# Optimization experiments

Hardware: AMD Instinct MI355X
Metric: run time of the kernel (lower is better)

Reference implementation:

```python
import jax, jax.numpy as jnp
import numpy as np

B, S, HID = 2, 2048, 2048
NH, NKV, HD = 16, 4, 128
EPS = 1e-6
THETA = 10000.0
NEG = jnp.float32(-1e30)


def setup_inputs() -> dict:
    key = jax.random.key(0)
    ks = jax.random.split(key, 7)
    return {
        "hidden_states": jax.random.normal(ks[0], (B, S, HID), jnp.float32) * 0.02,
        "positions": jnp.broadcast_to(jnp.arange(S, dtype=jnp.int32), (B, S)),
        "Wq": jax.random.normal(ks[1], (HID, NH * HD), jnp.float32) * (HID ** -0.5),
        "Wk": jax.random.normal(ks[2], (HID, NKV * HD), jnp.float32) * (HID ** -0.5),
        "Wv": jax.random.normal(ks[3], (HID, NKV * HD), jnp.float32) * (HID ** -0.5),
        "Wc": jax.random.normal(ks[4], (NH * HD, HID), jnp.float32) * ((NH * HD) ** -0.5),
        "q_scale": jax.random.uniform(ks[5], (HD,), jnp.float32),
        "k_scale": jax.random.uniform(ks[6], (HD,), jnp.float32),
    }


def _rmsnorm(x, scale):
    # per-head RMSNorm over head_dim (nnx.RMSNorm semantics)
    return x * jax.lax.rsqrt(jnp.mean(x * x, axis=-1, keepdims=True) + EPS) * scale


def _rope_neox(x, positions):
    # x: [B, S, H, HD]; full rotary_dim == HD, neox style (split halves)
    half = HD // 2
    inv_freq = 1.0 / (THETA ** (jnp.arange(half, dtype=jnp.float32) / half))
    ang = positions[..., None].astype(jnp.float32) * inv_freq  # [B, S, half]
    cos = jnp.cos(ang)[:, :, None, :]
    sin = jnp.sin(ang)[:, :, None, :]
    x1, x2 = jnp.split(x, 2, axis=-1)
    return jnp.concatenate([x1 * cos - x2 * sin, x2 * cos + x1 * sin], axis=-1)


def reference(hidden_states, positions, Wq, Wk, Wv, Wc, q_scale, k_scale):
    q = (hidden_states @ Wq).reshape(B, S, NH, HD)
    k = (hidden_states @ Wk).reshape(B, S, NKV, HD)
    v = (hidden_states @ Wv).reshape(B, S, NKV, HD)
    q = _rmsnorm(q, q_scale)
    k = _rmsnorm(k, k_scale)
    q = _rope_neox(q, positions)
    k = _rope_neox(k, positions)
    # GQA: expand KV heads to query heads
    rep = NH // NKV
    k = jnp.repeat(k, rep, axis=2)
    v = jnp.repeat(v, rep, axis=2)
    scores = jnp.einsum("bqhd,bkhd->bhqk", q, k) * (HD ** -0.5)
    causal = jnp.tril(jnp.ones((S, S), dtype=bool))
    scores = jnp.where(causal, scores, NEG)
    probs = jax.nn.softmax(scores, axis=-1)
    attn = jnp.einsum("bhqk,bkhd->bqhd", probs, v).reshape(B, S, NH * HD)
    return attn @ Wc
```

## Files before the change

kernel.cpp:

```cpp
#include <hip/hip_runtime.h>
#include <stdint.h>

typedef unsigned short u16;
typedef unsigned int u32;
typedef __bf16 bf16x8 __attribute__((ext_vector_type(8)));
typedef float f32x4 __attribute__((ext_vector_type(4)));
typedef u32 u32x4 __attribute__((ext_vector_type(4)));

__device__ __forceinline__ u16 f2bf(float x){
  u32 u = __float_as_uint(x);
  u += 0x7FFFu + ((u >> 16) & 1u);
  return (u16)(u >> 16);
}
__device__ __forceinline__ float bf2f(u16 h){
  return __uint_as_float(((u32)h) << 16);
}
__device__ __forceinline__ u32 cvt_pk_bf16(float lo, float hi){
  u32 r;
  asm("v_cvt_pk_bf16_f32 %0, %1, %2" : "=v"(r) : "v"(lo), "v"(hi));
  return r;
}
__device__ __forceinline__ f32x4 mfma16(bf16x8 a, bf16x8 b, f32x4 c){
  return __builtin_amdgcn_mfma_f32_16x16x32_bf16(a, b, c, 0, 0, 0);
}
__device__ __forceinline__ void gload16(const void* g, const void* l){
  __builtin_amdgcn_global_load_lds(
      (__attribute__((address_space(1))) void*)(uintptr_t)g,
      (__attribute__((address_space(3))) void*)(u32)(uintptr_t)l,
      16, 0, 0);
}

__global__ void k_rope_table(float* __restrict__ ct, float* __restrict__ st){
  int idx = blockIdx.x * 256 + threadIdx.x;
  int p = idx >> 6, i = idx & 63;
  float freq = powf(10000.0f, -(float)i / 64.0f);
  float ang = (float)p * freq;
  ct[idx] = cosf(ang);
  st[idx] = sinf(ang);
}

__global__ void k_cast_bf16(const float* __restrict__ in, u16* __restrict__ out){
  int i = (blockIdx.x * 256 + threadIdx.x) * 4;
  float4 v = *(const float4*)(in + i);
  ushort4 o;
  o.x = f2bf(v.x); o.y = f2bf(v.y); o.z = f2bf(v.z); o.w = f2bf(v.w);
  *(ushort4*)(out + i) = o;
}

__global__ void k_trans_qkv(const float* __restrict__ Wq, const float* __restrict__ Wk,
                            const float* __restrict__ Wv, u16* __restrict__ out){
  __shared__ float tile[32][33];
  int nb = blockIdx.x * 32, kb = blockIdx.y * 32;
  int tx = threadIdx.x, ty = threadIdx.y;
  #pragma unroll
  for (int j = 0; j < 4; j++){
    int k = kb + ty + j*8;
    int n = nb + tx;
    float v;
    if (n < 2048)      v = Wq[(size_t)k*2048 + n];
    else if (n < 2560) v = Wk[(size_t)k*512 + (n - 2048)];
    else               v = Wv[(size_t)k*512 + (n - 2560)];
    tile[tx][ty + j*8] = v;
  }
  __syncthreads();
  #pragma unroll
  for (int j = 0; j < 4; j++){
    int n = nb + ty + j*8;
    out[(size_t)n*2048 + kb + tx] = f2bf(tile[ty + j*8][tx]);
  }
}

__global__ void k_trans_wc(const float* __restrict__ Wc, u16* __restrict__ out){
  __shared__ float tile[32][33];
  int nb = blockIdx.x * 32, kb = blockIdx.y * 32;
  int tx = threadIdx.x, ty = threadIdx.y;
  #pragma unroll
  for (int j = 0; j < 4; j++){
    tile[tx][ty + j*8] = Wc[(size_t)(kb + ty + j*8)*2048 + nb + tx];
  }
  __syncthreads();
  #pragma unroll
  for (int j = 0; j < 4; j++){
    out[(size_t)(nb + ty + j*8)*2048 + kb + tx] = f2bf(tile[ty + j*8][tx]);
  }
}

template<bool OBF>
__global__ __launch_bounds__(256) void k_gemm(const u16* __restrict__ A, const u16* __restrict__ Bt,
                                              void* __restrict__ Cv, int M, int N, int K, int nbx){
  __shared__ u16 As[2][128*32], Bs[2][128*32];
  int tid = threadIdx.x;
  int lane = tid & 63, w = tid >> 6;
  int g = lane >> 4, c16 = lane & 15;
  int wr = w >> 1, wc = w & 1;
  int chunk = gridDim.x >> 3;
  int logical = (blockIdx.x & 7) * chunk + (blockIdx.x >> 3);
  int bx = logical % nbx, by = logical / nbx;
  size_t bm = (size_t)by * 128, bn = (size_t)bx * 128;
  f32x4 zero = {0.f, 0.f, 0.f, 0.f};
  f32x4 acc[4][4];
  #pragma unroll
  for (int i=0;i<4;i++)
    #pragma unroll
    for (int j=0;j<4;j++) acc[i][j] = zero;

  int jj = (w*2)*64 + lane;
  int nt = K >> 5;
  #pragma unroll
  for (int p = 0; p < 2; p++){
    int j = jj + p*64;
    int r = j >> 2, slot = j & 3;
    gload16(A  + (bm + r)*(size_t)K + slot*8, (const char*)As[0] + (w*2+p)*1024);
    gload16(Bt + (bn + r)*(size_t)K + slot*8, (const char*)Bs[0] + (w*2+p)*1024);
  }
  asm volatile("s_waitcnt vmcnt(0)" ::: "memory");
  __builtin_amdgcn_s_barrier();

  int cur = 0;
  for (int t = 0; t < nt; ++t){
    if (t + 1 < nt){
      int k0 = (t + 1) << 5;
      #pragma unroll
      for (int p = 0; p < 2; p++){
        int j = jj + p*64;
        int r = j >> 2, slot = j & 3;
        gload16(A  + (bm + r)*(size_t)K + k0 + slot*8, (const char*)As[cur^1] + (w*2+p)*1024);
        gload16(Bt + (bn + r)*(size_t)K + k0 + slot*8, (const char*)Bs[cur^1] + (w*2+p)*1024);
      }
    }
    const u16* Ac = As[cur];
    const u16* Bc = Bs[cur];
    bf16x8 af[4], bfr[4];
    #pragma unroll
    for (int mi=0;mi<4;mi++) af[mi]  = *(const bf16x8*)&Ac[(wr*64 + mi*16 + c16)*32 + g*8];
    #pragma unroll
    for (int ni=0;ni<4;ni++) bfr[ni] = *(const bf16x8*)&Bc[(wc*64 + ni*16 + c16)*32 + g*8];
    #pragma unroll
    for (int mi=0;mi<4;mi++)
      #pragma unroll
      for (int ni=0;ni<4;ni++)
        acc[mi][ni] = mfma16(af[mi], bfr[ni], acc[mi][ni]);
    if (t + 1 < nt){
      asm volatile("s_waitcnt vmcnt(0)" ::: "memory");
      __builtin_amdgcn_s_barrier();
    }
    cur ^= 1;
  }
  #pragma unroll
  for (int mi=0;mi<4;mi++){
    #pragma unroll
    for (int ni=0;ni<4;ni++){
      #pragma unroll
      for (int r=0;r<4;r++){
        size_t row = bm + wr*64 + mi*16 + g*4 + r;
        size_t col = bn + wc*64 + ni*16 + c16;
        if (OBF) ((u16*)Cv)[row * (size_t)N + col] = f2bf(acc[mi][ni][r]);
        else     ((float*)Cv)[row * (size_t)N + col] = acc[mi][ni][r];
      }
    }
  }
}

__global__ __launch_bounds__(256) void k_norm_rope(const u16* __restrict__ qkv, const int* __restrict__ pos,
    const float* __restrict__ qsc, const float* __restrict__ ksc,
    const float* __restrict__ ct, const float* __restrict__ st,
    u16* __restrict__ qo, u16* __restrict__ ko){
  int bs = blockIdx.x;
  int hh = blockIdx.y * 4 + (threadIdx.x >> 6);
  int d = threadIdx.x & 63;
  int b = bs >> 11, s = bs & 2047;
  const u16* row = qkv + (size_t)bs * 3072 + hh * 128;
  u16 r1 = row[d], r2 = row[d + 64];
  float x1 = bf2f(r1), x2 = bf2f(r2);
  float ssq = x1*x1 + x2*x2;
  #pragma unroll
  for (int mm = 1; mm < 64; mm <<= 1) ssq += __shfl_xor(ssq, mm);
  float inv = rsqrtf(ssq * (1.0f/128.0f) + 1e-6f);
  const float* sc = (hh < 16) ? qsc : ksc;
  float y1 = x1 * inv * sc[d];
  float y2 = x2 * inv * sc[d + 64];
  int p = pos[bs];
  float c = ct[p*64 + d], sn = st[p*64 + d];
  float o1 = y1*c - y2*sn;
  float o2 = y2*c + y1*sn;
  if (hh < 16){
    o1 *= 0.08838834764831845f;
    o2 *= 0.08838834764831845f;
    size_t o = ((size_t)(b*16 + hh) * 2048 + s) * 128 + d;
    qo[o] = f2bf(o1); qo[o + 64] = f2bf(o2);
  } else {
    size_t o = ((size_t)(b*4 + (hh-16)) * 2048 + s) * 128 + d;
    ko[o] = f2bf(o1); ko[o + 64] = f2bf(o2);
  }
}

__global__ __launch_bounds__(256) void k_vtrans(const u16* __restrict__ qkv, u16* __restrict__ vt){
  __shared__ u16 tile[64][132];
  int s0 = blockIdx.x * 64, kvh = blockIdx.y, b = blockIdx.z;
  int t = threadIdx.x;
  int r = t >> 2, qd = (t & 3) * 32;
  const u16* src = qkv + ((size_t)(b*2048 + s0 + r)) * 3072 + 2560 + kvh*128 + qd;
  #pragma unroll
  for (int i = 0; i < 4; i++)
    *(uint4*)&tile[r][qd + i*8] = *(const uint4*)(src + i*8);
  __syncthreads();
  int d = t >> 1, c = (t & 1) * 32;
  u16* dst = vt + ((size_t)(b*4 + kvh) * 128 + d) * 2048 + s0 + c;
  #pragma unroll
  for (int i = 0; i < 4; i++){
    u16 tmp[8];
    #pragma unroll
    for (int j = 0; j < 8; j++) tmp[j] = tile[c + i*8 + j][d];
    *(uint4*)(dst + i*8) = *(const uint4*)tmp;
  }
}

__device__ __forceinline__ void stage_kv(int w, int lane, u16* ksb, u16* vsb,
                                         const u16* kp, const u16* vp, int c0){
  #pragma unroll
  for (int p = 0; p < 4; p++){
    int j = (w*4 + p)*64 + lane;
    int r = j >> 4, slot = j & 15;
    const u16* src = kp + (size_t)(c0 + r)*128 + ((slot ^ (r & 7)) << 3);
    gload16(src, (const char*)ksb + (w*4 + p)*1024);
  }
  #pragma unroll
  for (int p = 0; p < 4; p++){
    int j = (w*4 + p)*64 + lane;
    int r = j >> 3, slot = j & 7;
    const u16* src = vp + (size_t)r*2048 + c0 + ((slot ^ (r & 7)) << 3);
    gload16(src, (const char*)vsb + (w*4 + p)*1024);
  }
}

__device__ __forceinline__ void proc_group(f32x4 (&sacc)[4], float &m, float &l,
    f32x4 (&o)[8], int qrow, bool diag, int c0, int lane, int g, int c16,
    const u16* vsb){
  if (diag){
    #pragma unroll
    for (int nt = 0; nt < 4; nt++)
      #pragma unroll
      for (int r = 0; r < 4; r++)
        if (c0 + nt*16 + g*4 + r > qrow) sacc[nt][r] = -1e30f;
  }
  float mx = fmaxf(fmaxf(sacc[0][0], sacc[0][1]), fmaxf(sacc[0][2], sacc[0][3]));
  #pragma unroll
  for (int nt = 1; nt < 4; nt++)
    mx = fmaxf(mx, fmaxf(fmaxf(sacc[nt][0], sacc[nt][1]), fmaxf(sacc[nt][2], sacc[nt][3])));
  mx = fmaxf(mx, __shfl_xor(mx, 16));
  mx = fmaxf(mx, __shfl_xor(mx, 32));
  if (__any(mx > m + 8.f)){
    float mn = fmaxf(m, mx);
    float al = __expf(m - mn);
    m = mn; l *= al;
    float alr[4];
    #pragma unroll
    for (int r = 0; r < 4; r++) alr[r] = __shfl(al, (lane & 48) | (g*4 + r));
    #pragma unroll
    for (int dt = 0; dt < 8; dt++)
      #pragma unroll
      for (int r = 0; r < 4; r++) o[dt][r] *= alr[r];
  }
  float s = 0.f;
  #pragma unroll
  for (int nt = 0; nt < 4; nt++)
    #pragma unroll
    for (int r = 0; r < 4; r++){
      float p = __expf(sacc[nt][r] - m);
      sacc[nt][r] = p;
      s += p;
    }
  s += __shfl_xor(s, 16);
  s += __shfl_xor(s, 32);
  l += s;
  u32 pkA[4], pkB[4];
  #pragma unroll
  for (int a = 0; a < 4; a++){
    pkA[a] = cvt_pk_bf16(sacc[a][0], sacc[a][1]);
    pkB[a] = cvt_pk_bf16(sacc[a][2], sacc[a][3]);
  }
  int s0l = (((g*2    ) & 3) << 4) | c16;
  int s1l = (((g*2 + 1) & 3) << 4) | c16;
  bool hi = (g & 2) != 0;
  u32 v0A[4], v0B[4], v1A[4], v1B[4];
  #pragma unroll
  for (int a = 0; a < 4; a++){
    v0A[a] = (u32)__shfl((int)pkA[a], s0l);
    v0B[a] = (u32)__shfl((int)pkB[a], s0l);
    v1A[a] = (u32)__shfl((int)pkA[a], s1l);
    v1B[a] = (u32)__shfl((int)pkB[a], s1l);
  }
  __builtin_amdgcn_s_setprio(1);
  #pragma unroll
  for (int kk2 = 0; kk2 < 2; kk2++){
    u32x4 pw;
    pw.x = hi ? v0A[2*kk2+1] : v0A[2*kk2];
    pw.y = hi ? v0B[2*kk2+1] : v0B[2*kk2];
    pw.z = hi ? v1A[2*kk2+1] : v1A[2*kk2];
    pw.w = hi ? v1B[2*kk2+1] : v1B[2*kk2];
    bf16x8 pf = __builtin_bit_cast(bf16x8, pw);
    #pragma unroll
    for (int dt = 0; dt < 8; dt++){
      int d = dt*16 + c16;
      bf16x8 vf = *(const bf16x8*)&vsb[d*64 + (((kk2*4 + g) ^ (d & 7)) << 3)];
      o[dt] = mfma16(pf, vf, o[dt]);
    }
  }
  __builtin_amdgcn_s_setprio(0);
}

__global__ __launch_bounds__(256, 2) void k_attn(const u16* __restrict__ q, const u16* __restrict__ k,
    const u16* __restrict__ vt, u16* __restrict__ attn){
  __shared__ u16 Ks[2][64*128];
  __shared__ u16 Vs[2][128*64];
  int lane = threadIdx.x & 63, w = threadIdx.x >> 6;
  int g = lane >> 4, c16 = lane & 15;
  int bid = blockIdx.x;
  int logical = (bid & 7)*64 + (bid >> 3);
  int pi = logical & 15;
  int hb = logical >> 4;
  int h = hb & 15, b = hb >> 4;
  int kvh = h >> 2;
  int qbA = pi*64, qbB = (31 - pi)*64;
  int tmax = 31 - pi;
  const u16* qp = q  + ((size_t)(b*16 + h))  * 2048 * 128;
  const u16* kp = k  + ((size_t)(b*4 + kvh)) * 2048 * 128;
  const u16* vp = vt + ((size_t)(b*4 + kvh)) * 128 * 2048;

  int qrA = qbA + w*16 + c16, qrB = qbB + w*16 + c16;
  bf16x8 qfA[4], qfB[4];
  #pragma unroll
  for (int kk = 0; kk < 4; kk++){
    qfA[kk] = *(const bf16x8*)(qp + (size_t)qrA*128 + kk*32 + g*8);
    qfB[kk] = *(const bf16x8*)(qp + (size_t)qrB*128 + kk*32 + g*8);
  }
  asm volatile("s_waitcnt vmcnt(0)" ::: "memory");

  f32x4 zero = {0.f,0.f,0.f,0.f};
  f32x4 oA[8], oB[8];
  #pragma unroll
  for (int i=0;i<8;i++){ oA[i] = zero; oB[i] = zero; }
  float mA = -1e30f, mB = -1e30f, lA = 0.f, lB = 0.f;

  stage_kv(w, lane, Ks[0], Vs[0], kp, vp, 0);

  for (int t = 0; t <= tmax; t++){
    int c0 = t*64;
    if (t < tmax){
      stage_kv(w, lane, Ks[(t+1)&1], Vs[(t+1)&1], kp, vp, c0 + 64);
      asm volatile("s_waitcnt vmcnt(8)" ::: "memory");
    } else {
      asm volatile("s_waitcnt vmcnt(0)" ::: "memory");
    }
    __builtin_amdgcn_s_barrier();
    const u16* ksb = Ks[t&1];
    const u16* vsb = Vs[t&1];
    bool Aact = (t <= pi);
    f32x4 sA[4], sB[4];
    #pragma unroll
    for (int i=0;i<4;i++){ sA[i] = zero; sB[i] = zero; }
    __builtin_amdgcn_s_setprio(1);
    if (Aact){
      #pragma unroll
      for (int nt=0;nt<4;nt++){
        #pragma unroll
        for (int kk=0;kk<4;kk++){
          int row = nt*16 + c16;
          bf16x8 kf = *(const bf16x8*)&ksb[row*128 + (((kk*4 + g) ^ (row & 7)) << 3)];
          sB[nt] = mfma16(kf, qfB[kk], sB[nt]);
          sA[nt] = mfma16(kf, qfA[kk], sA[nt]);
        }
      }
    } else {
      #pragma unroll
      for (int nt=0;nt<4;nt++){
        #pragma unroll
        for (int kk=0;kk<4;kk++){
          int row = nt*16 + c16;
          bf16x8 kf = *(const bf16x8*)&ksb[row*128 + (((kk*4 + g) ^ (row & 7)) << 3)];
          sB[nt] = mfma16(kf, qfB[kk], sB[nt]);
        }
      }
    }
    __builtin_amdgcn_s_setprio(0);
    if (Aact) proc_group(sA, mA, lA, oA, qrA, t == pi, c0, lane, g, c16, vsb);
    proc_group(sB, mB, lB, oB, qrB, t == tmax, c0, lane, g, c16, vsb);
    __builtin_amdgcn_sched_barrier(0);
    asm volatile("s_waitcnt lgkmcnt(0)" ::: "memory");
    __builtin_amdgcn_s_barrier();
  }
  float lrA[4], lrB[4];
  #pragma unroll
  for (int r = 0; r < 4; r++){
    lrA[r] = __shfl(lA, (lane & 48) | (g*4 + r));
    lrB[r] = __shfl(lB, (lane & 48) | (g*4 + r));
  }
  #pragma unroll
  for (int dt=0;dt<8;dt++){
    #pragma unroll
    for (int r=0;r<4;r++){
      size_t orA = (size_t)b*2048 + qbA + w*16 + g*4 + r;
      size_t orB = (size_t)b*2048 + qbB + w*16 + g*4 + r;
      attn[orA*2048 + (size_t)h*128 + dt*16 + c16] = f2bf(oA[dt][r] / lrA[r]);
      attn[orB*2048 + (size_t)h*128 + dt*16 + c16] = f2bf(oB[dt][r] / lrB[r]);
    }
  }
}

extern "C" void kernel_launch(void* const* d_in, const int* in_sizes, int n_in,
                              void* d_out, int out_size, void* d_ws, size_t ws_size,
                              hipStream_t stream){
  const float* hidden    = (const float*)d_in[0];
  const int*   positions = (const int*)d_in[1];
  const float* Wq = (const float*)d_in[2];
  const float* Wk = (const float*)d_in[3];
  const float* Wv = (const float*)d_in[4];
  const float* Wc = (const float*)d_in[5];
  const float* qs = (const float*)d_in[6];
  const float* ks = (const float*)d_in[7];
  float* out = (float*)d_out;
  char* ws = (char*)d_ws;
  float* ct      = (float*)(ws + 0);
  float* st      = (float*)(ws + 524288);
  u16*   hid_bf  = (u16*)(ws + 1048576);
  u16*   attn_bf = hid_bf;
  u16*   wqkv_t  = (u16*)(ws + 17825792);
  u16*   wct     = (u16*)(ws + 30408704);
  u16*   qkv_bf  = (u16*)(ws + 38797312);
  u16*   q_bf    = (u16*)(ws + 63963136);
  u16*   k_bf    = (u16*)(ws + 80740352);
  u16*   vt_bf   = (u16*)(ws + 84934656);

  k_rope_table<<<512, 256, 0, stream>>>(ct, st);
  k_cast_bf16<<<8192, 256, 0, stream>>>(hidden, hid_bf);
  k_trans_qkv<<<dim3(96, 64), dim3(32, 8), 0, stream>>>(Wq, Wk, Wv, wqkv_t);
  k_trans_wc<<<dim3(64, 64), dim3(32, 8), 0, stream>>>(Wc, wct);
  k_gemm<true><<<768, 256, 0, stream>>>(hid_bf, wqkv_t, (void*)qkv_bf, 4096, 3072, 2048, 24);
  k_norm_rope<<<dim3(4096, 5), 256, 0, stream>>>(qkv_bf, positions, qs, ks, ct, st, q_bf, k_bf);
  k_vtrans<<<dim3(32, 4, 2), 256, 0, stream>>>(qkv_bf, vt_bf);
  k_attn<<<512, 256, 0, stream>>>(q_bf, k_bf, vt_bf, attn_bf);
  k_gemm<false><<<512, 256, 0, stream>>>(attn_bf, wct, (void*)out, 4096, 2048, 2048, 16);
}
```

Measured before the change: 222.2 us.

## Merge prep kernels, split attention into single-tile blocks, use exp2 softmax

Four preprocessing kernels (rope table, hidden cast, two weight transposes) become one launch that dispatches on block index. The attention kernel drops the paired-tile layout, where each block handled q-tiles pi and 31-pi, and instead runs one 64-row q-tile per block over twice as many blocks. V gets a single buffer loaded separately from K, with an extra barrier before the PV step. Softmax switches to exp2 with the log2(e) factor folded into the Q scale, and the rescale threshold moves from 8 to 11.5. One-tile blocks give up the built-in causal load balancing and the sharing of K reads across two q tiles, and the single V buffer adds a wait inside each iteration.

```diff
diff --git a/kernel.cpp b/kernel.cpp
--- a/kernel.cpp
+++ b/kernel.cpp
@@ -30,58 +30,66 @@
       16, 0, 0);
 }
 
-__global__ void k_rope_table(float* __restrict__ ct, float* __restrict__ st){
-  int idx = blockIdx.x * 256 + threadIdx.x;
-  int p = idx >> 6, i = idx & 63;
-  float freq = powf(10000.0f, -(float)i / 64.0f);
-  float ang = (float)p * freq;
-  ct[idx] = cosf(ang);
-  st[idx] = sinf(ang);
-}
-
-__global__ void k_cast_bf16(const float* __restrict__ in, u16* __restrict__ out){
-  int i = (blockIdx.x * 256 + threadIdx.x) * 4;
-  float4 v = *(const float4*)(in + i);
-  ushort4 o;
-  o.x = f2bf(v.x); o.y = f2bf(v.y); o.z = f2bf(v.z); o.w = f2bf(v.w);
-  *(ushort4*)(out + i) = o;
-}
-
-__global__ void k_trans_qkv(const float* __restrict__ Wq, const float* __restrict__ Wk,
-                            const float* __restrict__ Wv, u16* __restrict__ out){
+__global__ __launch_bounds__(256) void k_prep(const float* __restrict__ hidden,
+    const float* __restrict__ Wq, const float* __restrict__ Wk, const float* __restrict__ Wv,
+    const float* __restrict__ Wc, u16* __restrict__ hid_bf, u16* __restrict__ wqkv_t,
+    u16* __restrict__ wct, float* __restrict__ ct, float* __restrict__ st){
   __shared__ float tile[32][33];
-  int nb = blockIdx.x * 32, kb = blockIdx.y * 32;
-  int tx = threadIdx.x, ty = threadIdx.y;
-  #pragma unroll
-  for (int j = 0; j < 4; j++){
-    int k = kb + ty + j*8;
-    int n = nb + tx;
-    float v;
-    if (n < 2048)      v = Wq[(size_t)k*2048 + n];
-    else if (n < 2560) v = Wk[(size_t)k*512 + (n - 2048)];
-    else               v = Wv[(size_t)k*512 + (n - 2560)];
-    tile[tx][ty + j*8] = v;
-  }
-  __syncthreads();
-  #pragma unroll
-  for (int j = 0; j < 4; j++){
-    int n = nb + ty + j*8;
-    out[(size_t)n*2048 + kb + tx] = f2bf(tile[ty + j*8][tx]);
-  }
-}
-
-__global__ void k_trans_wc(const float* __restrict__ Wc, u16* __restrict__ out){
-  __shared__ float tile[32][33];
-  int nb = blockIdx.x * 32, kb = blockIdx.y * 32;
-  int tx = threadIdx.x, ty = threadIdx.y;
-  #pragma unroll
-  for (int j = 0; j < 4; j++){
-    tile[tx][ty + j*8] = Wc[(size_t)(kb + ty + j*8)*2048 + nb + tx];
-  }
-  __syncthreads();
-  #pragma unroll
-  for (int j = 0; j < 4; j++){
-    out[(size_t)(nb + ty + j*8)*2048 + kb + tx] = f2bf(tile[ty + j*8][tx]);
+  int bid = blockIdx.x;
+  int t = threadIdx.x;
+  if (bid < 8192){
+    int i = (bid * 256 + t) * 4;
+    float4 v = *(const float4*)(hidden + i);
+    ushort4 o;
+    o.x = f2bf(v.x); o.y = f2bf(v.y); o.z = f2bf(v.z); o.w = f2bf(v.w);
+    *(ushort4*)(hid_bf + i) = o;
+    return;
+  }
+  if (bid < 8192 + 6144){
+    int b2 = bid - 8192;
+    int nb = (b2 % 96) * 32, kb = (b2 / 96) * 32;
+    int tx = t & 31, ty = t >> 5;
+    #pragma unroll
+    for (int j = 0; j < 4; j++){
+      int k = kb + ty + j*8;
+      int n = nb + tx;
+      float v;
+      if (n < 2048)      v = Wq[(size_t)k*2048 + n];
+      else if (n < 2560) v = Wk[(size_t)k*512 + (n - 2048)];
+      else               v = Wv[(size_t)k*512 + (n - 2560)];
+      tile[tx][ty + j*8] = v;
+    }
+    __syncthreads();
+    #pragma unroll
+    for (int j = 0; j < 4; j++){
+      int n = nb + ty + j*8;
+      wqkv_t[(size_t)n*2048 + kb + tx] = f2bf(tile[ty + j*8][tx]);
+    }
+    return;
+  }
+  if (bid < 8192 + 6144 + 4096){
+    int b3 = bid - 8192 - 6144;
+    int nb = (b3 % 64) * 32, kb = (b3 / 64) * 32;
+    int tx = t & 31, ty = t >> 5;
+    #pragma unroll
+    for (int j = 0; j < 4; j++){
+      tile[tx][ty + j*8] = Wc[(size_t)(kb + ty + j*8)*2048 + nb + tx];
+    }
+    __syncthreads();
+    #pragma unroll
+    for (int j = 0; j < 4; j++){
+      wct[(size_t)(nb + ty + j*8)*2048 + kb + tx] = f2bf(tile[ty + j*8][tx]);
+    }
+    return;
+  }
+  {
+    int b4 = bid - 8192 - 6144 - 4096;
+    int idx = b4 * 256 + t;
+    int p = idx >> 6, i = idx & 63;
+    float freq = powf(10000.0f, -(float)i / 64.0f);
+    float ang = (float)p * freq;
+    ct[idx] = cosf(ang);
+    st[idx] = sinf(ang);
   }
 }
 
@@ -184,8 +192,8 @@
   float o1 = y1*c - y2*sn;
   float o2 = y2*c + y1*sn;
   if (hh < 16){
-    o1 *= 0.08838834764831845f;
-    o2 *= 0.08838834764831845f;
+    o1 *= 0.1275174528f;
+    o2 *= 0.1275174528f;
     size_t o = ((size_t)(b*16 + hh) * 2048 + s) * 128 + d;
     qo[o] = f2bf(o1); qo[o + 64] = f2bf(o2);
   } else {
@@ -215,8 +223,7 @@
   }
 }
 
-__device__ __forceinline__ void stage_kv(int w, int lane, u16* ksb, u16* vsb,
-                                         const u16* kp, const u16* vp, int c0){
+__device__ __forceinline__ void stage_k(int w, int lane, u16* ksb, const u16* kp, int c0){
   #pragma unroll
   for (int p = 0; p < 4; p++){
     int j = (w*4 + p)*64 + lane;
@@ -224,6 +231,8 @@
     const u16* src = kp + (size_t)(c0 + r)*128 + ((slot ^ (r & 7)) << 3);
     gload16(src, (const char*)ksb + (w*4 + p)*1024);
   }
+}
+__device__ __forceinline__ void stage_v(int w, int lane, u16* vsb, const u16* vp, int c0){
   #pragma unroll
   for (int p = 0; p < 4; p++){
     int j = (w*4 + p)*64 + lane;
@@ -233,176 +242,146 @@
   }
 }
 
-__device__ __forceinline__ void proc_group(f32x4 (&sacc)[4], float &m, float &l,
-    f32x4 (&o)[8], int qrow, bool diag, int c0, int lane, int g, int c16,
-    const u16* vsb){
-  if (diag){
-    #pragma unroll
-    for (int nt = 0; nt < 4; nt++)
-      #pragma unroll
-      for (int r = 0; r < 4; r++)
-        if (c0 + nt*16 + g*4 + r > qrow) sacc[nt][r] = -1e30f;
-  }
-  float mx = fmaxf(fmaxf(sacc[0][0], sacc[0][1]), fmaxf(sacc[0][2], sacc[0][3]));
-  #pragma unroll
-  for (int nt = 1; nt < 4; nt++)
-    mx = fmaxf(mx, fmaxf(fmaxf(sacc[nt][0], sacc[nt][1]), fmaxf(sacc[nt][2], sacc[nt][3])));
-  mx = fmaxf(mx, __shfl_xor(mx, 16));
-  mx = fmaxf(mx, __shfl_xor(mx, 32));
-  if (__any(mx > m + 8.f)){
-    float mn = fmaxf(m, mx);
-    float al = __expf(m - mn);
-    m = mn; l *= al;
-    float alr[4];
-    #pragma unroll
-    for (int r = 0; r < 4; r++) alr[r] = __shfl(al, (lane & 48) | (g*4 + r));
-    #pragma unroll
-    for (int dt = 0; dt < 8; dt++)
-      #pragma unroll
-      for (int r = 0; r < 4; r++) o[dt][r] *= alr[r];
-  }
-  float s = 0.f;
-  #pragma unroll
-  for (int nt = 0; nt < 4; nt++)
-    #pragma unroll
-    for (int r = 0; r < 4; r++){
-      float p = __expf(sacc[nt][r] - m);
-      sacc[nt][r] = p;
-      s += p;
-    }
-  s += __shfl_xor(s, 16);
-  s += __shfl_xor(s, 32);
-  l += s;
-  u32 pkA[4], pkB[4];
-  #pragma unroll
-  for (int a = 0; a < 4; a++){
-    pkA[a] = cvt_pk_bf16(sacc[a][0], sacc[a][1]);
-    pkB[a] = cvt_pk_bf16(sacc[a][2], sacc[a][3]);
-  }
-  int s0l = (((g*2    ) & 3) << 4) | c16;
-  int s1l = (((g*2 + 1) & 3) << 4) | c16;
-  bool hi = (g & 2) != 0;
-  u32 v0A[4], v0B[4], v1A[4], v1B[4];
-  #pragma unroll
-  for (int a = 0; a < 4; a++){
-    v0A[a] = (u32)__shfl((int)pkA[a], s0l);
-    v0B[a] = (u32)__shfl((int)pkB[a], s0l);
-    v1A[a] = (u32)__shfl((int)pkA[a], s1l);
-    v1B[a] = (u32)__shfl((int)pkB[a], s1l);
-  }
-  __builtin_amdgcn_s_setprio(1);
-  #pragma unroll
-  for (int kk2 = 0; kk2 < 2; kk2++){
-    u32x4 pw;
-    pw.x = hi ? v0A[2*kk2+1] : v0A[2*kk2];
-    pw.y = hi ? v0B[2*kk2+1] : v0B[2*kk2];
-    pw.z = hi ? v1A[2*kk2+1] : v1A[2*kk2];
-    pw.w = hi ? v1B[2*kk2+1] : v1B[2*kk2];
-    bf16x8 pf = __builtin_bit_cast(bf16x8, pw);
-    #pragma unroll
-    for (int dt = 0; dt < 8; dt++){
-      int d = dt*16 + c16;
-      bf16x8 vf = *(const bf16x8*)&vsb[d*64 + (((kk2*4 + g) ^ (d & 7)) << 3)];
-      o[dt] = mfma16(pf, vf, o[dt]);
-    }
-  }
-  __builtin_amdgcn_s_setprio(0);
-}
-
 __global__ __launch_bounds__(256, 2) void k_attn(const u16* __restrict__ q, const u16* __restrict__ k,
     const u16* __restrict__ vt, u16* __restrict__ attn){
   __shared__ u16 Ks[2][64*128];
-  __shared__ u16 Vs[2][128*64];
+  __shared__ u16 Vs[128*64];
   int lane = threadIdx.x & 63, w = threadIdx.x >> 6;
   int g = lane >> 4, c16 = lane & 15;
   int bid = blockIdx.x;
-  int logical = (bid & 7)*64 + (bid >> 3);
-  int pi = logical & 15;
-  int hb = logical >> 4;
+  int logical = (bid & 7)*128 + (bid >> 3);
+  int hb = logical >> 5, qi = logical & 31;
   int h = hb & 15, b = hb >> 4;
   int kvh = h >> 2;
-  int qbA = pi*64, qbB = (31 - pi)*64;
-  int tmax = 31 - pi;
   const u16* qp = q  + ((size_t)(b*16 + h))  * 2048 * 128;
   const u16* kp = k  + ((size_t)(b*4 + kvh)) * 2048 * 128;
   const u16* vp = vt + ((size_t)(b*4 + kvh)) * 128 * 2048;
 
-  int qrA = qbA + w*16 + c16, qrB = qbB + w*16 + c16;
-  bf16x8 qfA[4], qfB[4];
-  #pragma unroll
-  for (int kk = 0; kk < 4; kk++){
-    qfA[kk] = *(const bf16x8*)(qp + (size_t)qrA*128 + kk*32 + g*8);
-    qfB[kk] = *(const bf16x8*)(qp + (size_t)qrB*128 + kk*32 + g*8);
-  }
+  int qrow = qi*64 + w*16 + c16;
+  bf16x8 qf[4];
+  #pragma unroll
+  for (int kk = 0; kk < 4; kk++)
+    qf[kk] = *(const bf16x8*)(qp + (size_t)qrow*128 + kk*32 + g*8);
   asm volatile("s_waitcnt vmcnt(0)" ::: "memory");
 
   f32x4 zero = {0.f,0.f,0.f,0.f};
-  f32x4 oA[8], oB[8];
-  #pragma unroll
-  for (int i=0;i<8;i++){ oA[i] = zero; oB[i] = zero; }
-  float mA = -1e30f, mB = -1e30f, lA = 0.f, lB = 0.f;
-
-  stage_kv(w, lane, Ks[0], Vs[0], kp, vp, 0);
-
-  for (int t = 0; t <= tmax; t++){
+  f32x4 o[8];
+  #pragma unroll
+  for (int i=0;i<8;i++) o[i] = zero;
+  float m = -1e30f, l = 0.f;
+
+  stage_k(w, lane, Ks[0], kp, 0);
+
+  for (int t = 0; t <= qi; t++){
     int c0 = t*64;
-    if (t < tmax){
-      stage_kv(w, lane, Ks[(t+1)&1], Vs[(t+1)&1], kp, vp, c0 + 64);
-      asm volatile("s_waitcnt vmcnt(8)" ::: "memory");
-    } else {
-      asm volatile("s_waitcnt vmcnt(0)" ::: "memory");
-    }
+    stage_v(w, lane, Vs, vp, c0);
+    if (t < qi) stage_k(w, lane, Ks[(t+1)&1], kp, c0 + 64);
+    if (t < qi) asm volatile("s_waitcnt vmcnt(8)" ::: "memory");
+    else        asm volatile("s_waitcnt vmcnt(4)" ::: "memory");
     __builtin_amdgcn_s_barrier();
     const u16* ksb = Ks[t&1];
-    const u16* vsb = Vs[t&1];
-    bool Aact = (t <= pi);
-    f32x4 sA[4], sB[4];
-    #pragma unroll
-    for (int i=0;i<4;i++){ sA[i] = zero; sB[i] = zero; }
+    f32x4 sacc[4];
+    #pragma unroll
+    for (int i=0;i<4;i++) sacc[i] = zero;
     __builtin_amdgcn_s_setprio(1);
-    if (Aact){
-      #pragma unroll
-      for (int nt=0;nt<4;nt++){
+    #pragma unroll
+    for (int nt=0;nt<4;nt++){
+      #pragma unroll
+      for (int kk=0;kk<4;kk++){
+        int row = nt*16 + c16;
+        bf16x8 kf = *(const bf16x8*)&ksb[row*128 + (((kk*4 + g) ^ (row & 7)) << 3)];
+        sacc[nt] = mfma16(kf, qf[kk], sacc[nt]);
+      }
+    }
+    __builtin_amdgcn_s_setprio(0);
+    if (t == qi){
+      #pragma unroll
+      for (int nt = 0; nt < 4; nt++)
         #pragma unroll
-        for (int kk=0;kk<4;kk++){
-          int row = nt*16 + c16;
-          bf16x8 kf = *(const bf16x8*)&ksb[row*128 + (((kk*4 + g) ^ (row & 7)) << 3)];
-          sB[nt] = mfma16(kf, qfB[kk], sB[nt]);
-          sA[nt] = mfma16(kf, qfA[kk], sA[nt]);
-        }
+        for (int r = 0; r < 4; r++)
+          if (c0 + nt*16 + g*4 + r > qrow) sacc[nt][r] = -1e30f;
+    }
+    float mx = fmaxf(fmaxf(sacc[0][0], sacc[0][1]), fmaxf(sacc[0][2], sacc[0][3]));
+    #pragma unroll
+    for (int nt = 1; nt < 4; nt++)
+      mx = fmaxf(mx, fmaxf(fmaxf(sacc[nt][0], sacc[nt][1]), fmaxf(sacc[nt][2], sacc[nt][3])));
+    mx = fmaxf(mx, __shfl_xor(mx, 16));
+    mx = fmaxf(mx, __shfl_xor(mx, 32));
+    if (__any(mx > m + 11.5f)){
+      float mn = fmaxf(m, mx);
+      float al = exp2f(m - mn);
+      m = mn; l *= al;
+      float alr[4];
+      #pragma unroll
+      for (int r = 0; r < 4; r++) alr[r] = __shfl(al, (lane & 48) | (g*4 + r));
+      #pragma unroll
+      for (int dt = 0; dt < 8; dt++)
+        #pragma unroll
+        for (int r = 0; r < 4; r++) o[dt][r] *= alr[r];
+    }
+    float s = 0.f;
+    #pragma unroll
+    for (int nt = 0; nt < 4; nt++)
+      #pragma unroll
+      for (int r = 0; r < 4; r++){
+        float p = exp2f(sacc[nt][r] - m);
+        sacc[nt][r] = p;
+        s += p;
       }
-    } else {
-      #pragma unroll
-      for (int nt=0;nt<4;nt++){
-        #pragma unroll
-        for (int kk=0;kk<4;kk++){
-          int row = nt*16 + c16;
-          bf16x8 kf = *(const bf16x8*)&ksb[row*128 + (((kk*4 + g) ^ (row & 7)) << 3)];
-          sB[nt] = mfma16(kf, qfB[kk], sB[nt]);
-        }
+    s += __shfl_xor(s, 16);
+    s += __shfl_xor(s, 32);
+    l += s;
+    u32 pkA[4], pkB[4];
+    #pragma unroll
+    for (int a = 0; a < 4; a++){
+      pkA[a] = cvt_pk_bf16(sacc[a][0], sacc[a][1]);
+      pkB[a] = cvt_pk_bf16(sacc[a][2], sacc[a][3]);
+    }
+    int s0l = (((g*2    ) & 3) << 4) | c16;
+    int s1l = (((g*2 + 1) & 3) << 4) | c16;
+    bool hi = (g & 2) != 0;
+    u32 v0A[4], v0B[4], v1A[4], v1B[4];
+    #pragma unroll
+    for (int a = 0; a < 4; a++){
+      v0A[a] = (u32)__shfl((int)pkA[a], s0l);
+      v0B[a] = (u32)__shfl((int)pkB[a], s0l);
+      v1A[a] = (u32)__shfl((int)pkA[a], s1l);
+      v1B[a] = (u32)__shfl((int)pkB[a], s1l);
+    }
+    if (t < qi) asm volatile("s_waitcnt vmcnt(4)" ::: "memory");
+    else        asm volatile("s_waitcnt vmcnt(0)" ::: "memory");
+    __builtin_amdgcn_s_barrier();
+    __builtin_amdgcn_s_setprio(1);
+    #pragma unroll
+    for (int kk2 = 0; kk2 < 2; kk2++){
+      u32x4 pw;
+      pw.x = hi ? v0A[2*kk2+1] : v0A[2*kk2];
+      pw.y = hi ? v0B[2*kk2+1] : v0B[2*kk2];
+      pw.z = hi ? v1A[2*kk2+1] : v1A[2*kk2];
+      pw.w = hi ? v1B[2*kk2+1] : v1B[2*kk2];
+      bf16x8 pf = __builtin_bit_cast(bf16x8, pw);
+      #pragma unroll
+      for (int dt = 0; dt < 8; dt++){
+        int d = dt*16 + c16;
+        bf16x8 vf = *(const bf16x8*)&Vs[d*64 + (((kk2*4 + g) ^ (d & 7)) << 3)];
+        o[dt] = mfma16(pf, vf, o[dt]);
       }
     }
     __builtin_amdgcn_s_setprio(0);
-    if (Aact) proc_group(sA, mA, lA, oA, qrA, t == pi, c0, lane, g, c16, vsb);
-    proc_group(sB, mB, lB, oB, qrB, t == tmax, c0, lane, g, c16, vsb);
     __builtin_amdgcn_sched_barrier(0);
     asm volatile("s_waitcnt lgkmcnt(0)" ::: "memory");
     __builtin_amdgcn_s_barrier();
   }
-  float lrA[4], lrB[4];
-  #pragma unroll
-  for (int r = 0; r < 4; r++){
-    lrA[r] = __shfl(lA, (lane & 48) | (g*4 + r));
-    lrB[r] = __shfl(lB, (lane & 48) | (g*4 + r));
-  }
+  float lr[4];
+  #pragma unroll
+  for (int r = 0; r < 4; r++)
+    lr[r] = __shfl(l, (lane & 48) | (g*4 + r));
   #pragma unroll
   for (int dt=0;dt<8;dt++){
     #pragma unroll
     for (int r=0;r<4;r++){
-      size_t orA = (size_t)b*2048 + qbA + w*16 + g*4 + r;
-      size_t orB = (size_t)b*2048 + qbB + w*16 + g*4 + r;
-      attn[orA*2048 + (size_t)h*128 + dt*16 + c16] = f2bf(oA[dt][r] / lrA[r]);
-      attn[orB*2048 + (size_t)h*128 + dt*16 + c16] = f2bf(oB[dt][r] / lrB[r]);
+      size_t orow = (size_t)b*2048 + qi*64 + w*16 + g*4 + r;
+      attn[orow*2048 + (size_t)h*128 + dt*16 + c16] = f2bf(o[dt][r] / lr[r]);
     }
   }
 }
@@ -431,13 +410,10 @@
   u16*   k_bf    = (u16*)(ws + 80740352);
   u16*   vt_bf   = (u16*)(ws + 84934656);
 
-  k_rope_table<<<512, 256, 0, stream>>>(ct, st);
-  k_cast_bf16<<<8192, 256, 0, stream>>>(hidden, hid_bf);
-  k_trans_qkv<<<dim3(96, 64), dim3(32, 8), 0, stream>>>(Wq, Wk, Wv, wqkv_t);
-  k_trans_wc<<<dim3(64, 64), dim3(32, 8), 0, stream>>>(Wc, wct);
+  k_prep<<<18944, 256, 0, stream>>>(hidden, Wq, Wk, Wv, Wc, hid_bf, wqkv_t, wct, ct, st);
   k_gemm<true><<<768, 256, 0, stream>>>(hid_bf, wqkv_t, (void*)qkv_bf, 4096, 3072, 2048, 24);
   k_norm_rope<<<dim3(4096, 5), 256, 0, stream>>>(qkv_bf, positions, qs, ks, ct, st, q_bf, k_bf);
   k_vtrans<<<dim3(32, 4, 2), 256, 0, stream>>>(qkv_bf, vt_bf);
-  k_attn<<<512, 256, 0, stream>>>(q_bf, k_bf, vt_bf, attn_bf);
+  k_attn<<<1024, 256, 0, stream>>>(q_bf, k_bf, vt_bf, attn_bf);
   k_gemm<false><<<512, 256, 0, stream>>>(attn_bf, wct, (void*)out, 4096, 2048, 2048, 16);
 }
```

Result: slower. 234.3 us (+5.5%).
